# Kernel tuning notes

Hardware: AMD Instinct MI355X
Metric: run time of the kernel (lower is better)

Reference implementation:

```python
import jax, jax.numpy as jnp
import numpy as np

B, T, D = 2, 2048, 1024
NH = 16
HD = D // NH


def setup_inputs() -> dict:
    key = jax.random.key(0)
    ks = jax.random.split(key, 5)
    s = 0.02
    return {
        "x": jax.random.normal(ks[0], (B, T, D), dtype=jnp.float32),
        "Wq": jax.random.normal(ks[1], (D, D), dtype=jnp.float32) * s,
        "Wk": jax.random.normal(ks[2], (D, D), dtype=jnp.float32) * s,
        "Wv": jax.random.normal(ks[3], (D, D), dtype=jnp.float32) * s,
        "Wo": jax.random.normal(ks[4], (D, D), dtype=jnp.float32) * s,
        "bo": jnp.zeros((D,), dtype=jnp.float32),
    }


def reference(x, Wq, Wk, Wv, Wo, bo):
    b, t, _ = x.shape
    scale = HD ** -0.5
    # torch Linear: y = x @ W^T
    q = (x @ Wq.T).reshape(b, t, NH, HD)
    k = (x @ Wk.T).reshape(b, t, NH, HD)
    v = (x @ Wv.T).reshape(b, t, NH, HD)
    # scores: [b, nh, t, t]
    s = jnp.einsum("bqhd,bkhd->bhqk", q, k) * scale
    causal = jnp.tril(jnp.ones((t, t), dtype=bool))
    s = jnp.where(causal, s, -jnp.inf)
    p = jax.nn.softmax(s, axis=-1)
    o = jnp.einsum("bhqk,bkhd->bqhd", p, v).reshape(b, t, D)
    return o @ Wo.T + bo
```

## Files before the change

kernel.cpp:

```cpp
#include <hip/hip_runtime.h>


typedef __bf16 bf16x8 __attribute__((ext_vector_type(8)));
typedef float f32x4 __attribute__((ext_vector_type(4)));
typedef unsigned short ushortx8 __attribute__((ext_vector_type(8)));
typedef unsigned short ushortx4 __attribute__((ext_vector_type(4)));

#define T_SEQ 2048
#define NHEAD 16
#define HDIM 64
#define DMODEL 1024

__device__ inline unsigned short f2bf(float f) {
  unsigned int u = __builtin_bit_cast(unsigned int, f);
  unsigned int r = (u + 0x7fffu + ((u >> 16) & 1u)) >> 16;
  return (unsigned short)r;
}

__device__ inline void gl16(const unsigned short* g, unsigned short* l) {
  __builtin_amdgcn_global_load_lds(
      (const __attribute__((address_space(1))) unsigned int*)g,
      (__attribute__((address_space(3))) unsigned int*)l, 16, 0, 0);
}

__global__ void cast_all(const float* __restrict__ x, const float* __restrict__ w0,
                         const float* __restrict__ w1, const float* __restrict__ w2,
                         const float* __restrict__ w3, unsigned short* __restrict__ out) {
  const int NX = 2 * T_SEQ * DMODEL;
  int i = (blockIdx.x * 256 + threadIdx.x) * 4;
  const float* src;
  int off;
  if (i < NX) {
    src = x; off = i;
  } else {
    const int j = i - NX;
    const int sel = j >> 20;
    off = j & ((1 << 20) - 1);
    src = sel == 0 ? w0 : sel == 1 ? w1 : sel == 2 ? w2 : w3;
  }
  float4 v = *reinterpret_cast<const float4*>(src + off);
  ushortx4 o;
  o[0] = f2bf(v.x); o[1] = f2bf(v.y); o[2] = f2bf(v.z); o[3] = f2bf(v.w);
  *reinterpret_cast<ushortx4*>(out + i) = o;
}

__device__ __forceinline__ void gemm_core(
    const unsigned short* __restrict__ A, const unsigned short* __restrict__ Bw,
    int K, int m0, int n0, f32x4 acc[4][4]) {
  __shared__ unsigned short As[4096];
  __shared__ unsigned short Bs[4096];
  const int tid = threadIdx.x;
  const int lane = tid & 63, wid = tid >> 6;
  const int wr = wid >> 1, wc = wid & 1;
  const int lr = lane & 15, lg = lane >> 4;
  const int srow = tid >> 2;
  const int scs = ((tid & 3) ^ (srow & 3)) * 8;
  const unsigned short* ga0 = A + (size_t)(m0 + srow) * K + scs;
  const unsigned short* gb0 = Bw + (size_t)(n0 + srow) * K + scs;
  unsigned short* la0 = As + tid * 8;
  unsigned short* lb0 = Bs + tid * 8;
  const int rca = (lg ^ (lr & 3)) * 8;

  for (int k0 = 0; k0 < K; k0 += 32) {
    __syncthreads();
    gl16(ga0 + k0, la0);
    gl16(ga0 + (size_t)64 * K + k0, la0 + 2048);
    gl16(gb0 + k0, lb0);
    gl16(gb0 + (size_t)64 * K + k0, lb0 + 2048);
    __syncthreads();

    bf16x8 af[4], bfr[4];
#pragma unroll
    for (int t = 0; t < 4; ++t) {
      af[t]  = *reinterpret_cast<const bf16x8*>(&As[(wr * 64 + t * 16 + lr) * 32 + rca]);
      bfr[t] = *reinterpret_cast<const bf16x8*>(&Bs[(wc * 64 + t * 16 + lr) * 32 + rca]);
    }
#pragma unroll
    for (int mi = 0; mi < 4; ++mi)
#pragma unroll
      for (int ni = 0; ni < 4; ++ni)
        acc[mi][ni] = __builtin_amdgcn_mfma_f32_16x16x32_bf16(af[mi], bfr[ni], acc[mi][ni], 0, 0, 0);
  }
}

__device__ __forceinline__ void gemm_core_n64(
    const unsigned short* __restrict__ A, const unsigned short* __restrict__ Bw,
    int K, int m0, int n0, f32x4 acc[4][2]) {
  __shared__ unsigned short As[4096];
  __shared__ unsigned short Bs[2048];
  const int tid = threadIdx.x;
  const int lane = tid & 63, wid = tid >> 6;
  const int wr = wid >> 1, wc = wid & 1;
  const int lr = lane & 15, lg = lane >> 4;
  const int srow = tid >> 2;
  const int scs = ((tid & 3) ^ (srow & 3)) * 8;
  const unsigned short* ga0 = A + (size_t)(m0 + srow) * K + scs;
  const unsigned short* gb0 = Bw + (size_t)(n0 + srow) * K + scs;
  unsigned short* la0 = As + tid * 8;
  unsigned short* lb0 = Bs + tid * 8;
  const int rca = (lg ^ (lr & 3)) * 8;

  for (int k0 = 0; k0 < K; k0 += 32) {
    __syncthreads();
    gl16(ga0 + k0, la0);
    gl16(ga0 + (size_t)64 * K + k0, la0 + 2048);
    gl16(gb0 + k0, lb0);
    __syncthreads();

    bf16x8 af[4], bfr[2];
#pragma unroll
    for (int t = 0; t < 4; ++t)
      af[t] = *reinterpret_cast<const bf16x8*>(&As[(wr * 64 + t * 16 + lr) * 32 + rca]);
#pragma unroll
    for (int t = 0; t < 2; ++t)
      bfr[t] = *reinterpret_cast<const bf16x8*>(&Bs[(wc * 32 + t * 16 + lr) * 32 + rca]);
#pragma unroll
    for (int mi = 0; mi < 4; ++mi)
#pragma unroll
      for (int ni = 0; ni < 2; ++ni)
        acc[mi][ni] = __builtin_amdgcn_mfma_f32_16x16x32_bf16(af[mi], bfr[ni], acc[mi][ni], 0, 0, 0);
  }
}

__global__ __launch_bounds__(256) void gemm_qkv(
    const unsigned short* __restrict__ xb, const unsigned short* __restrict__ Wall,
    unsigned short* __restrict__ Qb, unsigned short* __restrict__ Kb,
    unsigned short* __restrict__ Vtb) {
  const int z = blockIdx.y;
  const int bid = blockIdx.x;
  int m0, n0;
  const unsigned short* A;
  const unsigned short* Bw;
  if (z < 2) {
    n0 = (bid & 7) * 128; m0 = (bid >> 3) * 128;
    A = xb; Bw = Wall + (size_t)z * (DMODEL * DMODEL);
  } else {
    m0 = (bid & 7) * 128; n0 = (bid >> 3) * 128;
    A = Wall + (size_t)2 * (DMODEL * DMODEL); Bw = xb;
  }
  f32x4 acc[4][4] = {};
  gemm_core(A, Bw, DMODEL, m0, n0, acc);

  const int tid = threadIdx.x, lane = tid & 63, wid = tid >> 6;
  const int wr = wid >> 1, wc = wid & 1, lr = lane & 15, lg = lane >> 4;
  const int mb = m0 + wr * 64, nb = n0 + wc * 64;
  const float scale = z == 0 ? 0.125f * 1.44269504089f : 1.0f;
#pragma unroll
  for (int mi = 0; mi < 4; ++mi)
#pragma unroll
    for (int ni = 0; ni < 4; ++ni) {
      const int col = nb + ni * 16 + lr;
#pragma unroll
      for (int j = 0; j < 4; ++j) {
        const int row = mb + mi * 16 + lg * 4 + j;
        const float v = acc[mi][ni][j] * scale;
        if (z < 2) {
          const int b = row >> 11, t = row & (T_SEQ - 1);
          const int h = col >> 6, d = col & (HDIM - 1);
          unsigned short* out = z == 0 ? Qb : Kb;
          out[(((size_t)(b * NHEAD + h) * T_SEQ + t) << 6) + d] = f2bf(v);
        } else {
          const int h = row >> 6, d = row & (HDIM - 1);
          const int b = col >> 11, tt = col & (T_SEQ - 1);
          const int nib = (tt >> 2) & 7;
          const int nib2 = ((nib & 3) << 1) | (nib >> 2);
          const int tp = (tt & ~31) | (nib2 << 2) | (tt & 3);
          Vtb[(((size_t)(b * NHEAD + h) * HDIM + d) << 11) + tp] = f2bf(v);
        }
      }
    }
}

__global__ __launch_bounds__(256) void gemm_proj(
    const unsigned short* __restrict__ Ob, const unsigned short* __restrict__ Wob,
    float* __restrict__ out, const float* __restrict__ bias) {
  const int m0 = blockIdx.y * 128, n0 = blockIdx.x * 64;
  f32x4 acc[4][2] = {};
  gemm_core_n64(Ob, Wob, DMODEL, m0, n0, acc);

  const int tid = threadIdx.x, lane = tid & 63, wid = tid >> 6;
  const int wr = wid >> 1, wc = wid & 1, lr = lane & 15, lg = lane >> 4;
  const int mb = m0 + wr * 64, nb = n0 + wc * 32;
#pragma unroll
  for (int mi = 0; mi < 4; ++mi)
#pragma unroll
    for (int ni = 0; ni < 2; ++ni) {
      const int col = nb + ni * 16 + lr;
      const float bv = bias[col];
#pragma unroll
      for (int j = 0; j < 4; ++j) {
        const int row = mb + mi * 16 + lg * 4 + j;
        out[(size_t)row * DMODEL + col] = acc[mi][ni][j] + bv;
      }
    }
}

__device__ __forceinline__ void attn_step(
    const unsigned short* Kslot, const unsigned short* Vslot,
    const int kh0, const int kh1, const int (&vo)[2],
    const bf16x8 (&qf)[2], f32x4 (&acc)[4], float& lrun,
    const bool domask, const int kb, const int q, const int lg) {
  f32x4 s[4] = {};
  __builtin_amdgcn_s_setprio(1);
#pragma unroll
  for (int c = 0; c < 4; ++c) {
    bf16x8 k0 = *reinterpret_cast<const bf16x8*>(&Kslot[kh0 + c * 1024]);
    bf16x8 k1 = *reinterpret_cast<const bf16x8*>(&Kslot[kh1 + c * 1024]);
    s[c] = __builtin_amdgcn_mfma_f32_16x16x32_bf16(k0, qf[0], s[c], 0, 0, 0);
    s[c] = __builtin_amdgcn_mfma_f32_16x16x32_bf16(k1, qf[1], s[c], 0, 0, 0);
  }
  __builtin_amdgcn_s_setprio(0);
  if (domask) {
#pragma unroll
    for (int c = 0; c < 4; ++c)
#pragma unroll
      for (int j = 0; j < 4; ++j) {
        const int k = kb + c * 16 + lg * 4 + j;
        if (k > q) s[c][j] = -INFINITY;
      }
  }
  float tsum = 0.f;
#pragma unroll
  for (int c = 0; c < 4; ++c)
#pragma unroll
    for (int j = 0; j < 4; ++j) {
      const float p = exp2f(s[c][j]);
      s[c][j] = p;
      tsum += p;
    }
  lrun += tsum;

  bf16x8 pb[2];
#pragma unroll
  for (int ks = 0; ks < 2; ++ks) {
    bf16x8 t8;
#pragma unroll
    for (int e = 0; e < 8; ++e) t8[e] = (__bf16)s[ks * 2 + (e >> 2)][e & 3];
    pb[ks] = t8;
  }
  __builtin_amdgcn_s_setprio(1);
#pragma unroll
  for (int dt = 0; dt < 4; ++dt)
#pragma unroll
    for (int ks = 0; ks < 2; ++ks) {
      bf16x8 vf = *reinterpret_cast<const bf16x8*>(&Vslot[vo[ks] + dt * 1024]);
      acc[dt] = __builtin_amdgcn_mfma_f32_16x16x32_bf16(vf, pb[ks], acc[dt], 0, 0, 0);
    }
  __builtin_amdgcn_s_setprio(0);
}

__global__ __launch_bounds__(512, 4) void flash_attn(
    const unsigned short* __restrict__ Q, const unsigned short* __restrict__ Kg,
    const unsigned short* __restrict__ Vt, unsigned short* __restrict__ O) {
  __shared__ unsigned short Ks[5][4096];
  __shared__ unsigned short Vs[5][4096];
  const int tid = threadIdx.x, lane = tid & 63, wid = tid >> 6;
  const int lr = lane & 15, lg = lane >> 4, wq = wid & 3;
  const int bid = blockIdx.x;
  const int bh = (bid & 7) * 4 + ((bid >> 3) & 3);
  const int a = (bid >> 5) & 15;
  const int b = 31 - a;
  const bool g0 = wid < 4;
  const int myq1 = g0 ? a : b;
  const int q1 = myq1 * 64 + wq * 16 + lr;
  const int q2 = b * 64 + wq * 16 + lr;
  const size_t base = (size_t)bh * (T_SEQ * HDIM);

  bf16x8 qf1[2], qf2[2];
#pragma unroll
  for (int h = 0; h < 2; ++h) {
    qf1[h] = *reinterpret_cast<const bf16x8*>(Q + base + (size_t)q1 * HDIM + h * 32 + lg * 8);
    qf2[h] = *reinterpret_cast<const bf16x8*>(Q + base + (size_t)q2 * HDIM + h * 32 + lg * 8);
  }

  const int srow = tid >> 3;
  const int schk = ((tid & 7) ^ (srow & 7)) * 8;
  const unsigned short* kst = Kg + base + (size_t)srow * HDIM + schk;
  const unsigned short* vst = Vt + base + (size_t)srow * T_SEQ + schk;

#define STAGE(slot, kt_)                                \
  do {                                                  \
    const int kb_ = (kt_) * 64;                         \
    gl16(kst + (size_t)kb_ * HDIM, &Ks[slot][tid * 8]); \
    gl16(vst + kb_, &Vs[slot][tid * 8]);                \
  } while (0)

  const int kh0 = lr * 64 + ((lg ^ (lr & 7)) * 8);
  const int kh1 = lr * 64 + (((4 + lg) ^ (lr & 7)) * 8);
  int vo[2];
#pragma unroll
  for (int ks = 0; ks < 2; ++ks)
    vo[ks] = lr * 64 + (((ks * 4 + lg) ^ (lr & 7)) * 8);

  float l1 = 0.f, l2 = 0.f;
  f32x4 acc1[4] = {}, acc2[4] = {};

  STAGE(0, 0);
  STAGE(1, 1);
  asm volatile("s_waitcnt vmcnt(2)" ::: "memory");
  __builtin_amdgcn_s_barrier();
  asm volatile("" ::: "memory");

  int sl = 0;
  for (int kt = 0; kt <= a; ++kt) {
    const int st = kt + 2;
    int sst = sl + 2; if (sst >= 5) sst -= 5;
    if (st <= b) STAGE(sst, st);
    attn_step(Ks[sl], Vs[sl], kh0, kh1, vo, qf1, acc1, l1,
              g0 && (kt == a), kt * 64, q1, lg);
    if (kt < a && st <= b) {
      asm volatile("s_waitcnt vmcnt(2)" ::: "memory");
    } else {
      asm volatile("s_waitcnt vmcnt(0)" ::: "memory");
    }
    __builtin_amdgcn_s_barrier();
    asm volatile("" ::: "memory");
    ++sl; if (sl >= 5) sl -= 5;
  }

  {
    int s3 = sl + 2; if (s3 >= 5) s3 -= 5;
    if (a + 3 <= b) STAGE(s3, a + 3);
  }
  for (int t0 = a + 1; t0 <= b; t0 += 2) {
    int s1 = sl + 1; if (s1 >= 5) s1 -= 5;
    int s3 = sl + 3; if (s3 >= 5) s3 -= 5;
    int s4 = sl + 4; if (s4 >= 5) s4 -= 5;
    if (t0 + 3 <= b) STAGE(s3, t0 + 3);
    if (t0 + 4 <= b) STAGE(s4, t0 + 4);
    if (!g0) {
      attn_step(Ks[sl], Vs[sl], kh0, kh1, vo, qf2, acc1, l1,
                t0 == b, t0 * 64, q2, lg);
    } else if (t0 + 1 <= b) {
      attn_step(Ks[s1], Vs[s1], kh0, kh1, vo, qf2, acc2, l2,
                false, (t0 + 1) * 64, q2, lg);
    }
    if (t0 + 4 <= b) {
      asm volatile("s_waitcnt vmcnt(2)" ::: "memory");
    } else {
      asm volatile("s_waitcnt vmcnt(0)" ::: "memory");
    }
    __builtin_amdgcn_s_barrier();
    asm volatile("" ::: "memory");
    sl += 2; if (sl >= 5) sl -= 5;
  }
#undef STAGE

  float* sm = reinterpret_cast<float*>(&Ks[0][0]);
  const int lid = (wq * 64 + lane) * 18;
  if (g0) {
    float* p = sm + lid;
    p[0] = l2;
#pragma unroll
    for (int dt = 0; dt < 4; ++dt)
#pragma unroll
      for (int j = 0; j < 4; ++j) p[2 + dt * 4 + j] = acc2[dt][j];
  }
  __syncthreads();
  if (!g0) {
    const float* p = sm + lid;
    l1 += p[0];
#pragma unroll
    for (int dt = 0; dt < 4; ++dt)
#pragma unroll
      for (int j = 0; j < 4; ++j)
        acc1[dt][j] += p[2 + dt * 4 + j];
  }

  l1 += __shfl_xor(l1, 16, 64);
  l1 += __shfl_xor(l1, 32, 64);

  const int b_ = bh >> 4, h_ = bh & (NHEAD - 1);
  const float inv = 1.0f / l1;
  unsigned short* orow = O + (((size_t)(b_ * T_SEQ + q1)) << 10) + h_ * HDIM + lg * 4;
#pragma unroll
  for (int dt = 0; dt < 4; ++dt) {
    ushortx4 o4;
#pragma unroll
    for (int j = 0; j < 4; ++j) o4[j] = f2bf(acc1[dt][j] * inv);
    *reinterpret_cast<ushortx4*>(orow + dt * 16) = o4;
  }
}

extern "C" void kernel_launch(void* const* d_in, const int* in_sizes, int n_in,
                              void* d_out, int out_size, void* d_ws, size_t ws_size,
                              hipStream_t stream) {
  const float* x  = (const float*)d_in[0];
  const float* Wq = (const float*)d_in[1];
  const float* Wk = (const float*)d_in[2];
  const float* Wv = (const float*)d_in[3];
  const float* Wo = (const float*)d_in[4];
  const float* bo = (const float*)d_in[5];
  float* out = (float*)d_out;

  const int M = 2 * T_SEQ;
  const int NXD = DMODEL * DMODEL;
  const int NX = M * DMODEL;

  unsigned short* ws = (unsigned short*)d_ws;
  unsigned short* xb  = ws;
  unsigned short* Wqb = xb + NX;
  unsigned short* Wob = Wqb + 3 * (size_t)NXD;
  unsigned short* Qb  = Wqb + 4 * (size_t)NXD;
  unsigned short* Kbf = Qb + NX;
  unsigned short* Vtb = Kbf + NX;
  unsigned short* Ob  = Vtb + NX;

  cast_all<<<(NX + 4 * NXD) / 1024, 256, 0, stream>>>(x, Wq, Wk, Wv, Wo, xb);

  dim3 gq(256, 3);
  gemm_qkv<<<gq, 256, 0, stream>>>(xb, Wqb, Qb, Kbf, Vtb);

  flash_attn<<<512, 512, 0, stream>>>(Qb, Kbf, Vtb, Ob);

  dim3 gg(DMODEL / 64, M / 128);
  gemm_proj<<<gg, 256, 0, stream>>>(Ob, Wob, out, bo);
}
```

Baseline: 100.2 us.

## Software-pipeline QK^T across iterations and compute row sums via MFMA with ones

```diff
diff --git a/kernel.cpp b/kernel.cpp
--- a/kernel.cpp
+++ b/kernel.cpp
@@ -195,10 +195,40 @@
     }
 }
 
+__device__ __forceinline__ void sm_pack(f32x4 (&s)[4], bf16x8 (&pb)[2]) {
+#pragma unroll
+  for (int c = 0; c < 4; ++c)
+#pragma unroll
+    for (int j = 0; j < 4; ++j) s[c][j] = exp2f(s[c][j]);
+#pragma unroll
+  for (int ks = 0; ks < 2; ++ks) {
+    bf16x8 t8;
+#pragma unroll
+    for (int e = 0; e < 8; ++e) t8[e] = (__bf16)s[ks * 2 + (e >> 2)][e & 3];
+    pb[ks] = t8;
+  }
+}
+
+__device__ __forceinline__ void pv_acc(
+    const unsigned short* Vslot, const int (&vo)[2], const bf16x8 (&pb)[2],
+    f32x4 (&acc)[4], f32x4& lacc, const bf16x8 ones) {
+  __builtin_amdgcn_s_setprio(1);
+#pragma unroll
+  for (int dt = 0; dt < 4; ++dt)
+#pragma unroll
+    for (int ks = 0; ks < 2; ++ks) {
+      bf16x8 vf = *reinterpret_cast<const bf16x8*>(&Vslot[vo[ks] + dt * 1024]);
+      acc[dt] = __builtin_amdgcn_mfma_f32_16x16x32_bf16(vf, pb[ks], acc[dt], 0, 0, 0);
+    }
+  lacc = __builtin_amdgcn_mfma_f32_16x16x32_bf16(ones, pb[0], lacc, 0, 0, 0);
+  lacc = __builtin_amdgcn_mfma_f32_16x16x32_bf16(ones, pb[1], lacc, 0, 0, 0);
+  __builtin_amdgcn_s_setprio(0);
+}
+
 __device__ __forceinline__ void attn_step(
     const unsigned short* Kslot, const unsigned short* Vslot,
     const int kh0, const int kh1, const int (&vo)[2],
-    const bf16x8 (&qf)[2], f32x4 (&acc)[4], float& lrun,
+    const bf16x8 (&qf)[2], f32x4 (&acc)[4], f32x4& lacc, const bf16x8 ones,
     const bool domask, const int kb, const int q, const int lg) {
   f32x4 s[4] = {};
   __builtin_amdgcn_s_setprio(1);
@@ -219,34 +249,9 @@
         if (k > q) s[c][j] = -INFINITY;
       }
   }
-  float tsum = 0.f;
-#pragma unroll
-  for (int c = 0; c < 4; ++c)
-#pragma unroll
-    for (int j = 0; j < 4; ++j) {
-      const float p = exp2f(s[c][j]);
-      s[c][j] = p;
-      tsum += p;
-    }
-  lrun += tsum;
-
   bf16x8 pb[2];
-#pragma unroll
-  for (int ks = 0; ks < 2; ++ks) {
-    bf16x8 t8;
-#pragma unroll
-    for (int e = 0; e < 8; ++e) t8[e] = (__bf16)s[ks * 2 + (e >> 2)][e & 3];
-    pb[ks] = t8;
-  }
-  __builtin_amdgcn_s_setprio(1);
-#pragma unroll
-  for (int dt = 0; dt < 4; ++dt)
-#pragma unroll
-    for (int ks = 0; ks < 2; ++ks) {
-      bf16x8 vf = *reinterpret_cast<const bf16x8*>(&Vslot[vo[ks] + dt * 1024]);
-      acc[dt] = __builtin_amdgcn_mfma_f32_16x16x32_bf16(vf, pb[ks], acc[dt], 0, 0, 0);
-    }
-  __builtin_amdgcn_s_setprio(0);
+  sm_pack(s, pb);
+  pv_acc(Vslot, vo, pb, acc, lacc, ones);
 }
 
 __global__ __launch_bounds__(512, 4) void flash_attn(
@@ -272,6 +277,9 @@
     qf1[h] = *reinterpret_cast<const bf16x8*>(Q + base + (size_t)q1 * HDIM + h * 32 + lg * 8);
     qf2[h] = *reinterpret_cast<const bf16x8*>(Q + base + (size_t)q2 * HDIM + h * 32 + lg * 8);
   }
+  bf16x8 ones;
+#pragma unroll
+  for (int e = 0; e < 8; ++e) ones[e] = (__bf16)1.0f;
 
   const int srow = tid >> 3;
   const int schk = ((tid & 7) ^ (srow & 7)) * 8;
@@ -292,23 +300,67 @@
   for (int ks = 0; ks < 2; ++ks)
     vo[ks] = lr * 64 + (((ks * 4 + lg) ^ (lr & 7)) * 8);
 
-  float l1 = 0.f, l2 = 0.f;
   f32x4 acc1[4] = {}, acc2[4] = {};
+  f32x4 lacc1 = {}, lacc2 = {};
 
   STAGE(0, 0);
   STAGE(1, 1);
+  STAGE(2, 2);
   asm volatile("s_waitcnt vmcnt(2)" ::: "memory");
   __builtin_amdgcn_s_barrier();
   asm volatile("" ::: "memory");
 
+  f32x4 sC[4];
+  {
+#pragma unroll
+    for (int c = 0; c < 4; ++c) {
+      bf16x8 k0 = *reinterpret_cast<const bf16x8*>(&Ks[0][kh0 + c * 1024]);
+      bf16x8 k1 = *reinterpret_cast<const bf16x8*>(&Ks[0][kh1 + c * 1024]);
+      f32x4 t = {};
+      t = __builtin_amdgcn_mfma_f32_16x16x32_bf16(k0, qf1[0], t, 0, 0, 0);
+      t = __builtin_amdgcn_mfma_f32_16x16x32_bf16(k1, qf1[1], t, 0, 0, 0);
+      sC[c] = t;
+    }
+  }
+
   int sl = 0;
   for (int kt = 0; kt <= a; ++kt) {
-    const int st = kt + 2;
-    int sst = sl + 2; if (sst >= 5) sst -= 5;
-    if (st <= b) STAGE(sst, st);
-    attn_step(Ks[sl], Vs[sl], kh0, kh1, vo, qf1, acc1, l1,
-              g0 && (kt == a), kt * 64, q1, lg);
-    if (kt < a && st <= b) {
+    int s1 = sl + 1; if (s1 >= 5) s1 -= 5;
+    int s3 = sl + 3; if (s3 >= 5) s3 -= 5;
+    if (kt + 3 <= b) STAGE(s3, kt + 3);
+    const bool pf = kt < a;
+    bf16x8 kfN[4][2];
+    if (pf) {
+#pragma unroll
+      for (int c = 0; c < 4; ++c) {
+        kfN[c][0] = *reinterpret_cast<const bf16x8*>(&Ks[s1][kh0 + c * 1024]);
+        kfN[c][1] = *reinterpret_cast<const bf16x8*>(&Ks[s1][kh1 + c * 1024]);
+      }
+    }
+    if (g0 && kt == a) {
+#pragma unroll
+      for (int c = 0; c < 4; ++c)
+#pragma unroll
+        for (int j = 0; j < 4; ++j) {
+          const int k = kt * 64 + c * 16 + lg * 4 + j;
+          if (k > q1) sC[c][j] = -INFINITY;
+        }
+    }
+    bf16x8 pb[2];
+    sm_pack(sC, pb);
+    if (pf) {
+      __builtin_amdgcn_s_setprio(1);
+#pragma unroll
+      for (int c = 0; c < 4; ++c) {
+        f32x4 t = {};
+        t = __builtin_amdgcn_mfma_f32_16x16x32_bf16(kfN[c][0], qf1[0], t, 0, 0, 0);
+        t = __builtin_amdgcn_mfma_f32_16x16x32_bf16(kfN[c][1], qf1[1], t, 0, 0, 0);
+        sC[c] = t;
+      }
+      __builtin_amdgcn_s_setprio(0);
+    }
+    pv_acc(Vs[sl], vo, pb, acc1, lacc1, ones);
+    if (kt < a) {
       asm volatile("s_waitcnt vmcnt(2)" ::: "memory");
     } else {
       asm volatile("s_waitcnt vmcnt(0)" ::: "memory");
@@ -318,10 +370,6 @@
     ++sl; if (sl >= 5) sl -= 5;
   }
 
-  {
-    int s3 = sl + 2; if (s3 >= 5) s3 -= 5;
-    if (a + 3 <= b) STAGE(s3, a + 3);
-  }
   for (int t0 = a + 1; t0 <= b; t0 += 2) {
     int s1 = sl + 1; if (s1 >= 5) s1 -= 5;
     int s3 = sl + 3; if (s3 >= 5) s3 -= 5;
@@ -329,10 +377,10 @@
     if (t0 + 3 <= b) STAGE(s3, t0 + 3);
     if (t0 + 4 <= b) STAGE(s4, t0 + 4);
     if (!g0) {
-      attn_step(Ks[sl], Vs[sl], kh0, kh1, vo, qf2, acc1, l1,
+      attn_step(Ks[sl], Vs[sl], kh0, kh1, vo, qf2, acc1, lacc1, ones,
                 t0 == b, t0 * 64, q2, lg);
     } else if (t0 + 1 <= b) {
-      attn_step(Ks[s1], Vs[s1], kh0, kh1, vo, qf2, acc2, l2,
+      attn_step(Ks[s1], Vs[s1], kh0, kh1, vo, qf2, acc2, lacc2, ones,
                 false, (t0 + 1) * 64, q2, lg);
     }
     if (t0 + 4 <= b) {
@@ -350,13 +398,14 @@
   const int lid = (wq * 64 + lane) * 18;
   if (g0) {
     float* p = sm + lid;
-    p[0] = l2;
+    p[0] = lacc2[0];
 #pragma unroll
     for (int dt = 0; dt < 4; ++dt)
 #pragma unroll
       for (int j = 0; j < 4; ++j) p[2 + dt * 4 + j] = acc2[dt][j];
   }
   __syncthreads();
+  float l1 = lacc1[0];
   if (!g0) {
     const float* p = sm + lid;
     l1 += p[0];
@@ -366,9 +415,6 @@
       for (int j = 0; j < 4; ++j)
         acc1[dt][j] += p[2 + dt * 4 + j];
   }
-
-  l1 += __shfl_xor(l1, 16, 64);
-  l1 += __shfl_xor(l1, 32, 64);
 
   const int b_ = bh >> 4, h_ = bh & (NHEAD - 1);
   const float inv = 1.0f / l1;
```

Measured after the change: 99.10 us, median of 3. Within noise of the previous version (-1.1%).

## Split flash attention into one query tile per block and compute row sums via MFMA

Applied to the files above, without the earlier changes.

```diff
diff --git a/kernel.cpp b/kernel.cpp
--- a/kernel.cpp
+++ b/kernel.cpp
@@ -3,7 +3,6 @@
 
 typedef __bf16 bf16x8 __attribute__((ext_vector_type(8)));
 typedef float f32x4 __attribute__((ext_vector_type(4)));
-typedef unsigned short ushortx8 __attribute__((ext_vector_type(8)));
 typedef unsigned short ushortx4 __attribute__((ext_vector_type(4)));
 
 #define T_SEQ 2048
@@ -198,7 +197,7 @@
 __device__ __forceinline__ void attn_step(
     const unsigned short* Kslot, const unsigned short* Vslot,
     const int kh0, const int kh1, const int (&vo)[2],
-    const bf16x8 (&qf)[2], f32x4 (&acc)[4], float& lrun,
+    const bf16x8 (&qf)[2], f32x4 (&acc)[4], f32x4& lacc, const bf16x8 ones,
     const bool domask, const int kb, const int q, const int lg) {
   f32x4 s[4] = {};
   __builtin_amdgcn_s_setprio(1);
@@ -219,17 +218,10 @@
         if (k > q) s[c][j] = -INFINITY;
       }
   }
-  float tsum = 0.f;
 #pragma unroll
   for (int c = 0; c < 4; ++c)
 #pragma unroll
-    for (int j = 0; j < 4; ++j) {
-      const float p = exp2f(s[c][j]);
-      s[c][j] = p;
-      tsum += p;
-    }
-  lrun += tsum;
-
+    for (int j = 0; j < 4; ++j) s[c][j] = exp2f(s[c][j]);
   bf16x8 pb[2];
 #pragma unroll
   for (int ks = 0; ks < 2; ++ks) {
@@ -246,32 +238,33 @@
       bf16x8 vf = *reinterpret_cast<const bf16x8*>(&Vslot[vo[ks] + dt * 1024]);
       acc[dt] = __builtin_amdgcn_mfma_f32_16x16x32_bf16(vf, pb[ks], acc[dt], 0, 0, 0);
     }
+  lacc = __builtin_amdgcn_mfma_f32_16x16x32_bf16(ones, pb[0], lacc, 0, 0, 0);
+  lacc = __builtin_amdgcn_mfma_f32_16x16x32_bf16(ones, pb[1], lacc, 0, 0, 0);
   __builtin_amdgcn_s_setprio(0);
 }
 
-__global__ __launch_bounds__(512, 4) void flash_attn(
+__global__ __launch_bounds__(512, 8) void flash_attn(
     const unsigned short* __restrict__ Q, const unsigned short* __restrict__ Kg,
     const unsigned short* __restrict__ Vt, unsigned short* __restrict__ O) {
-  __shared__ unsigned short Ks[5][4096];
-  __shared__ unsigned short Vs[5][4096];
+  __shared__ unsigned short Ks[4][4096];
+  __shared__ unsigned short Vs[4][4096];
   const int tid = threadIdx.x, lane = tid & 63, wid = tid >> 6;
   const int lr = lane & 15, lg = lane >> 4, wq = wid & 3;
+  const bool g0 = wid < 4;
   const int bid = blockIdx.x;
   const int bh = (bid & 7) * 4 + ((bid >> 3) & 3);
-  const int a = (bid >> 5) & 15;
-  const int b = 31 - a;
-  const bool g0 = wid < 4;
-  const int myq1 = g0 ? a : b;
-  const int q1 = myq1 * 64 + wq * 16 + lr;
-  const int q2 = b * 64 + wq * 16 + lr;
+  const int kk = (bid >> 5) & 7, seg = (bid >> 8) & 3;
+  const int qt = seg == 0 ? kk : seg == 1 ? 31 - kk : seg == 2 ? kk + 8 : 23 - kk;
+  const int q = qt * 64 + wq * 16 + lr;
   const size_t base = (size_t)bh * (T_SEQ * HDIM);
 
-  bf16x8 qf1[2], qf2[2];
-#pragma unroll
-  for (int h = 0; h < 2; ++h) {
-    qf1[h] = *reinterpret_cast<const bf16x8*>(Q + base + (size_t)q1 * HDIM + h * 32 + lg * 8);
-    qf2[h] = *reinterpret_cast<const bf16x8*>(Q + base + (size_t)q2 * HDIM + h * 32 + lg * 8);
-  }
+  bf16x8 qf[2];
+#pragma unroll
+  for (int h = 0; h < 2; ++h)
+    qf[h] = *reinterpret_cast<const bf16x8*>(Q + base + (size_t)q * HDIM + h * 32 + lg * 8);
+  bf16x8 ones;
+#pragma unroll
+  for (int e = 0; e < 8; ++e) ones[e] = (__bf16)1.0f;
 
   const int srow = tid >> 3;
   const int schk = ((tid & 7) ^ (srow & 7)) * 8;
@@ -292,93 +285,64 @@
   for (int ks = 0; ks < 2; ++ks)
     vo[ks] = lr * 64 + (((ks * 4 + lg) ^ (lr & 7)) * 8);
 
-  float l1 = 0.f, l2 = 0.f;
-  f32x4 acc1[4] = {}, acc2[4] = {};
+  f32x4 acc[4] = {};
+  f32x4 lacc = {};
+  const int nt = qt + 1;
+  const int ni = (nt + 1) >> 1;
 
   STAGE(0, 0);
-  STAGE(1, 1);
-  asm volatile("s_waitcnt vmcnt(2)" ::: "memory");
+  if (nt > 1) STAGE(1, 1);
+  asm volatile("s_waitcnt vmcnt(0)" ::: "memory");
   __builtin_amdgcn_s_barrier();
   asm volatile("" ::: "memory");
 
-  int sl = 0;
-  for (int kt = 0; kt <= a; ++kt) {
-    const int st = kt + 2;
-    int sst = sl + 2; if (sst >= 5) sst -= 5;
-    if (st <= b) STAGE(sst, st);
-    attn_step(Ks[sl], Vs[sl], kh0, kh1, vo, qf1, acc1, l1,
-              g0 && (kt == a), kt * 64, q1, lg);
-    if (kt < a && st <= b) {
-      asm volatile("s_waitcnt vmcnt(2)" ::: "memory");
-    } else {
-      asm volatile("s_waitcnt vmcnt(0)" ::: "memory");
-    }
+  for (int i = 0; i < ni; ++i) {
+    const int t0 = 2 * i, t1 = 2 * i + 1;
+    if (t0 + 2 < nt) STAGE((t0 + 2) & 3, t0 + 2);
+    if (t0 + 3 < nt) STAGE((t0 + 3) & 3, t0 + 3);
+    if (g0) {
+      attn_step(Ks[t0 & 3], Vs[t0 & 3], kh0, kh1, vo, qf, acc, lacc, ones,
+                t0 == qt, t0 * 64, q, lg);
+    } else if (t1 < nt) {
+      attn_step(Ks[t1 & 3], Vs[t1 & 3], kh0, kh1, vo, qf, acc, lacc, ones,
+                t1 == qt, t1 * 64, q, lg);
+    }
+    asm volatile("s_waitcnt vmcnt(0)" ::: "memory");
     __builtin_amdgcn_s_barrier();
     asm volatile("" ::: "memory");
-    ++sl; if (sl >= 5) sl -= 5;
-  }
-
-  {
-    int s3 = sl + 2; if (s3 >= 5) s3 -= 5;
-    if (a + 3 <= b) STAGE(s3, a + 3);
-  }
-  for (int t0 = a + 1; t0 <= b; t0 += 2) {
-    int s1 = sl + 1; if (s1 >= 5) s1 -= 5;
-    int s3 = sl + 3; if (s3 >= 5) s3 -= 5;
-    int s4 = sl + 4; if (s4 >= 5) s4 -= 5;
-    if (t0 + 3 <= b) STAGE(s3, t0 + 3);
-    if (t0 + 4 <= b) STAGE(s4, t0 + 4);
-    if (!g0) {
-      attn_step(Ks[sl], Vs[sl], kh0, kh1, vo, qf2, acc1, l1,
-                t0 == b, t0 * 64, q2, lg);
-    } else if (t0 + 1 <= b) {
-      attn_step(Ks[s1], Vs[s1], kh0, kh1, vo, qf2, acc2, l2,
-                false, (t0 + 1) * 64, q2, lg);
-    }
-    if (t0 + 4 <= b) {
-      asm volatile("s_waitcnt vmcnt(2)" ::: "memory");
-    } else {
-      asm volatile("s_waitcnt vmcnt(0)" ::: "memory");
-    }
-    __builtin_amdgcn_s_barrier();
-    asm volatile("" ::: "memory");
-    sl += 2; if (sl >= 5) sl -= 5;
   }
 #undef STAGE
 
   float* sm = reinterpret_cast<float*>(&Ks[0][0]);
   const int lid = (wq * 64 + lane) * 18;
+  if (!g0) {
+    float* p = sm + lid;
+    p[0] = lacc[0];
+#pragma unroll
+    for (int dt = 0; dt < 4; ++dt)
+#pragma unroll
+      for (int j = 0; j < 4; ++j) p[2 + dt * 4 + j] = acc[dt][j];
+  }
+  __syncthreads();
   if (g0) {
-    float* p = sm + lid;
-    p[0] = l2;
+    const float* p = sm + lid;
+    float l1 = lacc[0] + p[0];
 #pragma unroll
     for (int dt = 0; dt < 4; ++dt)
 #pragma unroll
-      for (int j = 0; j < 4; ++j) p[2 + dt * 4 + j] = acc2[dt][j];
-  }
-  __syncthreads();
-  if (!g0) {
-    const float* p = sm + lid;
-    l1 += p[0];
-#pragma unroll
-    for (int dt = 0; dt < 4; ++dt)
-#pragma unroll
       for (int j = 0; j < 4; ++j)
-        acc1[dt][j] += p[2 + dt * 4 + j];
-  }
-
-  l1 += __shfl_xor(l1, 16, 64);
-  l1 += __shfl_xor(l1, 32, 64);
-
-  const int b_ = bh >> 4, h_ = bh & (NHEAD - 1);
-  const float inv = 1.0f / l1;
-  unsigned short* orow = O + (((size_t)(b_ * T_SEQ + q1)) << 10) + h_ * HDIM + lg * 4;
-#pragma unroll
-  for (int dt = 0; dt < 4; ++dt) {
-    ushortx4 o4;
-#pragma unroll
-    for (int j = 0; j < 4; ++j) o4[j] = f2bf(acc1[dt][j] * inv);
-    *reinterpret_cast<ushortx4*>(orow + dt * 16) = o4;
+        acc[dt][j] += p[2 + dt * 4 + j];
+
+    const int b_ = bh >> 4, h_ = bh & (NHEAD - 1);
+    const float inv = 1.0f / l1;
+    unsigned short* orow = O + (((size_t)(b_ * T_SEQ + q)) << 10) + h_ * HDIM + lg * 4;
+#pragma unroll
+    for (int dt = 0; dt < 4; ++dt) {
+      ushortx4 o4;
+#pragma unroll
+      for (int j = 0; j < 4; ++j) o4[j] = f2bf(acc[dt][j] * inv);
+      *reinterpret_cast<ushortx4*>(orow + dt * 16) = o4;
+    }
   }
 }
 
@@ -411,7 +375,7 @@
   dim3 gq(256, 3);
   gemm_qkv<<<gq, 256, 0, stream>>>(xb, Wqb, Qb, Kbf, Vtb);
 
-  flash_attn<<<512, 512, 0, stream>>>(Qb, Kbf, Vtb, Ob);
+  flash_attn<<<1024, 512, 0, stream>>>(Qb, Kbf, Vtb, Ob);
 
   dim3 gg(DMODEL / 64, M / 128);
   gemm_proj<<<gg, 256, 0, stream>>>(Ob, Wob, out, bo);
```

After: 106.4 us. 6.2% more time.
